# Performance work log

Measured on AMD Instinct MI355X. Metric: run time of the kernel, lower is better.

Reference implementation:

```python
import jax, jax.numpy as jnp
import numpy as np

N_BONDS = 16777216
N_ATOMS = 1048576
N_TYPES = 16


def setup_inputs() -> dict:
    key = jax.random.key(0)
    k1, k2, k3, k4, k5, k6 = jax.random.split(key, 6)
    # bond orders kept strictly positive so BO**p_be2 and its grad are finite
    bo_sigma = jax.random.uniform(k1, (N_BONDS,), jnp.float32, 0.05, 1.0)
    bo_pi = jax.random.uniform(k2, (N_BONDS,), jnp.float32, 0.05, 1.0)
    bo_pipi = jax.random.uniform(k3, (N_BONDS,), jnp.float32, 0.05, 1.0)
    bond_type = jax.random.randint(k4, (N_BONDS,), 0, N_TYPES, jnp.int32)
    atom_i = jax.random.randint(k5, (N_BONDS,), 0, N_ATOMS, jnp.int32)
    # columns: De_sigma, De_pi, De_pipi, p_be1, p_be2 (positive, O(1))
    bond_params = jax.random.uniform(k6, (N_TYPES, 5), jnp.float32, 0.1, 1.0)
    return {
        "bond_type": bond_type,
        "atom_i": atom_i,
        "bo_sigma": bo_sigma,
        "bo_pi": bo_pi,
        "bo_pipi": bo_pipi,
        "bond_params": bond_params,
        "n_atoms": N_ATOMS,
    }


def reference(bond_type, atom_i, bo_sigma, bo_pi, bo_pipi, bond_params, n_atoms):
    # Gather per-bond-type parameters: [E, 5]
    p = bond_params[bond_type]
    de_s, de_p, de_pp, p_be1, p_be2 = (p[:, 0], p[:, 1], p[:, 2], p[:, 3], p[:, 4])
    # ReaxFF bond energy per bond
    e_bond = (-de_s * bo_sigma * jnp.exp(p_be1 * (1.0 - bo_sigma ** p_be2))
              - de_p * bo_pi
              - de_pp * bo_pipi)
    # Scatter-reduce to per-atom energy
    e_atom = jax.ops.segment_sum(e_bond, atom_i, num_segments=n_atoms)
    return e_atom
```

## Files before the change

kernel.cpp:

```cpp
#include <hip/hip_runtime.h>


typedef float    f32x4 __attribute__((ext_vector_type(4)));
typedef int      i32x4 __attribute__((ext_vector_type(4)));
typedef unsigned u32x4 __attribute__((ext_vector_type(4)));
typedef unsigned u32;

#define NBUK   64
#define RANGEK 16384
#define SHIFTK 14
#define CB     8192
#define TB     256
#define PADQ   8u
#define SPLITS 4

__device__ __forceinline__ u32 f32_to_bf16_bits(float f) {
    u32 u = __float_as_uint(f);
    return ((u + 0x7FFFu + ((u >> 16) & 1u)) >> 16) & 0xFFFFu;
}

__global__ __launch_bounds__(TB, 4) void partition_kernel(
        const i32x4* __restrict__ bt, const i32x4* __restrict__ ai,
        const f32x4* __restrict__ bs_, const f32x4* __restrict__ bp_,
        const f32x4* __restrict__ bpp_, const float* __restrict__ bond_params,
        u32* __restrict__ gcur, u32* __restrict__ arena,
        float* __restrict__ out, u32 slab, int round_start) {
    __shared__ u32   sorted[CB];
    __shared__ u32   hist[4][NBUK];
    __shared__ u32   start_[NBUK], cur[NBUK], graw_[NBUK], ovf_[NBUK];
    __shared__ float4 sp_a[16];
    __shared__ float  sp_b[16];

    int tid = threadIdx.x, sb = blockIdx.x;
    ((u32*)hist)[tid] = 0u;
    if (tid < 16) {
        const float* p = bond_params + tid * 5;
        sp_a[tid] = make_float4(p[0], p[1], p[2], p[3]);
        sp_b[tid] = p[4];
    }
    __syncthreads();

    long base4 = ((long)round_start + (long)sb * CB) >> 2;
    int w = tid >> 6;
    i32x4 av[CB / (TB * 4)];
#pragma unroll
    for (int it = 0; it < CB / (TB * 4); ++it) {
        av[it] = ai[base4 + it * TB + tid];
        atomicAdd(&hist[w][(u32)av[it].x >> SHIFTK], 1u);
        atomicAdd(&hist[w][(u32)av[it].y >> SHIFTK], 1u);
        atomicAdd(&hist[w][(u32)av[it].z >> SHIFTK], 1u);
        atomicAdd(&hist[w][(u32)av[it].w >> SHIFTK], 1u);
    }
    __syncthreads();

    if (tid < 64) {
        u32 c = hist[0][tid] + hist[1][tid] + hist[2][tid] + hist[3][tid];
        u32 s = c;
#pragma unroll
        for (int off = 1; off < 64; off <<= 1) {
            u32 n = __shfl_up(s, off);
            if (tid >= off) s += n;
        }
        start_[tid] = s - c;
        cur[tid]    = s - c;
        u32 plen = (c + PADQ - 1u) & ~(PADQ - 1u);
        u32 g = atomicAdd(&gcur[tid], plen);
        graw_[tid] = g;
        ovf_[tid]  = (g + plen > slab) ? 1u : 0u;
    }
    __syncthreads();

#pragma unroll
    for (int it = 0; it < CB / (TB * 4); ++it) {
        long idx = base4 + it * TB + tid;
        i32x4 t  = bt[idx];
        f32x4 s  = bs_[idx];
        f32x4 p  = bp_[idx];
        f32x4 pp = bpp_[idx];
        i32x4 a  = av[it];
#pragma unroll
        for (int k = 0; k < 4; ++k) {
            u32 ak = (u32)a[k];
            float4 pa = sp_a[t[k]];
            float  pb = sp_b[t[k]];
            float pw = __powf(s[k], pb);
            float e  = -pa.x * s[k] * __expf(pa.w * (1.0f - pw))
                       - pa.y * p[k] - pa.z * pp[k];
            u32 b = ak >> SHIFTK;
            u32 pos = atomicAdd(&cur[b], 1u);
            sorted[pos] = ((ak & (RANGEK - 1u)) << 16) | f32_to_bf16_bits(e);
        }
    }
    __syncthreads();

    int lane = tid & 63;
    for (int b = w; b < NBUK; b += 4) {
        u32 ls = start_[b], len = cur[b] - ls;
        u32 plen = (len + PADQ - 1u) & ~(PADQ - 1u);
        u32 g = graw_[b];
        if (!ovf_[b]) {
            size_t base = (size_t)b * slab + g;
            for (u32 j = lane; j < plen; j += 64u)
                arena[base + j] = (j < len) ? sorted[ls + j] : 0u;
        } else {
            u32 z0 = g < slab ? g : slab;
            u32 z1 = (g + plen) < slab ? (g + plen) : slab;
            for (u32 j = z0 + lane; j < z1; j += 64u)
                arena[(size_t)b * slab + j] = 0u;
            for (u32 j = lane; j < len; j += 64u) {
                u32 e = sorted[ls + j];
                unsafeAtomicAdd(&out[((u32)b << SHIFTK) + (e >> 16)],
                                __uint_as_float((e & 0xFFFFu) << 16));
            }
        }
    }
}

__global__ __launch_bounds__(1024) void accum_kernel(
        const u32* __restrict__ arena, const u32* __restrict__ gcur,
        float* __restrict__ partials, u32 slab) {
    __shared__ float acc[RANGEK];
    int tid = threadIdx.x;
    int b = blockIdx.x >> 2, sp = blockIdx.x & 3;
    f32x4* a4 = (f32x4*)acc;
#pragma unroll
    for (int i = 0; i < RANGEK / 4 / 1024; ++i)
        a4[i * 1024 + tid] = (f32x4)(0.f);
    __syncthreads();
    u32 n = gcur[b];
    if (n > slab) n = slab;
    u32 nv = n >> 2;
    const u32x4* src = (const u32x4*)(arena + (size_t)b * slab);
    for (u32 j = (u32)sp * 1024u + tid; j < nv; j += 4096u) {
        u32x4 e = __builtin_nontemporal_load(&src[j]);
        atomicAdd(&acc[e.x >> 16], __uint_as_float((e.x & 0xFFFFu) << 16));
        atomicAdd(&acc[e.y >> 16], __uint_as_float((e.y & 0xFFFFu) << 16));
        atomicAdd(&acc[e.z >> 16], __uint_as_float((e.z & 0xFFFFu) << 16));
        atomicAdd(&acc[e.w >> 16], __uint_as_float((e.w & 0xFFFFu) << 16));
    }
    __syncthreads();
    f32x4* pr = (f32x4*)(partials + ((size_t)sp * NBUK + b) * RANGEK);
#pragma unroll
    for (int i = 0; i < RANGEK / 4 / 1024; ++i)
        pr[i * 1024 + tid] = a4[i * 1024 + tid];
}

__global__ __launch_bounds__(TB) void merge_kernel(
        const float* __restrict__ partials, float* __restrict__ out,
        int n_atoms) {
    int i = blockIdx.x * TB + threadIdx.x;
    const f32x4* p0 = (const f32x4*)partials;
    const f32x4* p1 = (const f32x4*)(partials + (size_t)n_atoms);
    const f32x4* p2 = (const f32x4*)(partials + 2 * (size_t)n_atoms);
    const f32x4* p3 = (const f32x4*)(partials + 3 * (size_t)n_atoms);
    f32x4* o4 = (f32x4*)out;
    o4[i] += p0[i] + p1[i] + p2[i] + p3[i];
}

__global__ __launch_bounds__(TB) void zero_kernel(f32x4* __restrict__ p, int n4) {
    int i = blockIdx.x * blockDim.x + threadIdx.x;
    if (i < n4) p[i] = (f32x4)(0.f);
}

__global__ __launch_bounds__(TB) void atomic_fallback_kernel(
        const i32x4* __restrict__ bt, const i32x4* __restrict__ ai,
        const f32x4* __restrict__ bs_, const f32x4* __restrict__ bp_,
        const f32x4* __restrict__ bpp_, const float* __restrict__ bond_params,
        float* __restrict__ out, int n4) {
    __shared__ float sp[80];
    if (threadIdx.x < 80) sp[threadIdx.x] = bond_params[threadIdx.x];
    __syncthreads();
    int i = blockIdx.x * blockDim.x + threadIdx.x;
    if (i >= n4) return;
    i32x4 t  = bt[i]; i32x4 a = ai[i];
    f32x4 s  = bs_[i]; f32x4 p = bp_[i]; f32x4 pp = bpp_[i];
#pragma unroll
    for (int k = 0; k < 4; ++k) {
        const float* pr = sp + t[k] * 5;
        float pw = __powf(s[k], pr[4]);
        float e  = -pr[0] * s[k] * __expf(pr[3] * (1.0f - pw))
                   - pr[1] * p[k] - pr[2] * pp[k];
        unsafeAtomicAdd(&out[a[k]], e);
    }
}

extern "C" void kernel_launch(void* const* d_in, const int* in_sizes, int n_in,
                              void* d_out, int out_size, void* d_ws, size_t ws_size,
                              hipStream_t stream) {
    const int*   bond_type   = (const int*)  d_in[0];
    const int*   atom_i      = (const int*)  d_in[1];
    const float* bo_sigma    = (const float*)d_in[2];
    const float* bo_pi       = (const float*)d_in[3];
    const float* bo_pipi     = (const float*)d_in[4];
    const float* bond_params = (const float*)d_in[5];
    float*       e_atom      = (float*)d_out;

    const int n_bonds = in_sizes[0];
    const int n_atoms = out_size;

    int cfg_nr = 0; u32 cfg_slab = 0;
    if (n_atoms == (NBUK << SHIFTK)) {
        const int cands[5] = {1, 2, 4, 8, 16};
        for (int ci = 0; ci < 5 && !cfg_nr; ++ci) {
            int r = cands[ci];
            if (n_bonds % (r * CB)) continue;
            long cpr = (long)n_bonds / r, nsb = cpr / CB;
            if (nsb < 256 || nsb > 8192) continue;
            u32 sl = (u32)((cpr / NBUK + nsb * 4 + 8192 + 7) & ~7L);
            size_t need = (size_t)NBUK * sl * 4
                        + 1024
                        + (size_t)SPLITS * n_atoms * 4;
            if (need <= ws_size) { cfg_nr = r; cfg_slab = sl; }
        }
    }

    if (cfg_nr) {
        const int NR = cfg_nr, cpr = n_bonds / NR, nsb = cpr / CB;
        u32*   arena    = (u32*)d_ws;
        u32*   gcur     = arena + (size_t)NBUK * cfg_slab;
        float* partials = (float*)(gcur + 256);
        int zn4 = n_atoms / 4;
        zero_kernel<<<(zn4 + TB - 1) / TB, TB, 0, stream>>>((f32x4*)e_atom, zn4);
        for (int r = 0; r < NR; ++r) {
            int rs = r * cpr;
            hipMemsetAsync(gcur, 0, NBUK * sizeof(u32), stream);
            partition_kernel<<<nsb, TB, 0, stream>>>(
                (const i32x4*)bond_type, (const i32x4*)atom_i,
                (const f32x4*)bo_sigma, (const f32x4*)bo_pi, (const f32x4*)bo_pipi,
                bond_params, gcur, arena, e_atom, cfg_slab, rs);
            accum_kernel<<<NBUK * SPLITS, 1024, 0, stream>>>(
                arena, gcur, partials, cfg_slab);
            merge_kernel<<<n_atoms / 4 / TB, TB, 0, stream>>>(
                partials, e_atom, n_atoms);
        }
    } else {
        int zn4 = n_atoms / 4;
        zero_kernel<<<(zn4 + TB - 1) / TB, TB, 0, stream>>>((f32x4*)e_atom, zn4);
        int n4 = n_bonds / 4;
        atomic_fallback_kernel<<<(n4 + TB - 1) / TB, TB, 0, stream>>>(
            (const i32x4*)bond_type, (const i32x4*)atom_i,
            (const f32x4*)bo_sigma, (const f32x4*)bo_pi, (const f32x4*)bo_pipi,
            bond_params, e_atom, n4);
    }
}
```

Measured before the change: 437.8 us.

## Split histogram into count kernel and replace partials merge with direct atomics

Moves the per-block bucket histogram into a separate count pass that stores u16 counts, so the partition kernel no longer keeps atom indices in registers across phases. Partition loads all inputs with nontemporal hints. The accumulate kernel atomically adds its shared-memory accumulator straight into the output, which removes the partials buffer and the merge kernel. The cost is reading atom_i twice and an extra launch; slab padding is also reduced.

```diff
diff --git a/kernel.cpp b/kernel.cpp
--- a/kernel.cpp
+++ b/kernel.cpp
@@ -5,6 +5,7 @@
 typedef int      i32x4 __attribute__((ext_vector_type(4)));
 typedef unsigned u32x4 __attribute__((ext_vector_type(4)));
 typedef unsigned u32;
+typedef unsigned short u16;
 
 #define NBUK   64
 #define RANGEK 16384
@@ -19,42 +20,48 @@
     return ((u + 0x7FFFu + ((u >> 16) & 1u)) >> 16) & 0xFFFFu;
 }
 
+__global__ __launch_bounds__(TB) void count_kernel(
+        const i32x4* __restrict__ atom_i, u16* __restrict__ counts,
+        int round_start) {
+    __shared__ u32 hist[4][NBUK];
+    int tid = threadIdx.x, w = tid >> 6;
+    ((u32*)hist)[tid] = 0u;
+    __syncthreads();
+    long base4 = ((long)round_start + (long)blockIdx.x * CB) >> 2;
+#pragma unroll
+    for (int it = 0; it < CB / (TB * 4); ++it) {
+        i32x4 a = __builtin_nontemporal_load(&atom_i[base4 + it * TB + tid]);
+        atomicAdd(&hist[w][(u32)a.x >> SHIFTK], 1u);
+        atomicAdd(&hist[w][(u32)a.y >> SHIFTK], 1u);
+        atomicAdd(&hist[w][(u32)a.z >> SHIFTK], 1u);
+        atomicAdd(&hist[w][(u32)a.w >> SHIFTK], 1u);
+    }
+    __syncthreads();
+    if (tid < NBUK)
+        counts[(size_t)blockIdx.x * NBUK + tid] =
+            (u16)(hist[0][tid] + hist[1][tid] + hist[2][tid] + hist[3][tid]);
+}
+
 __global__ __launch_bounds__(TB, 4) void partition_kernel(
         const i32x4* __restrict__ bt, const i32x4* __restrict__ ai,
         const f32x4* __restrict__ bs_, const f32x4* __restrict__ bp_,
         const f32x4* __restrict__ bpp_, const float* __restrict__ bond_params,
-        u32* __restrict__ gcur, u32* __restrict__ arena,
-        float* __restrict__ out, u32 slab, int round_start) {
+        const u16* __restrict__ counts, u32* __restrict__ gcur,
+        u32* __restrict__ arena, float* __restrict__ out,
+        u32 slab, int round_start) {
     __shared__ u32   sorted[CB];
-    __shared__ u32   hist[4][NBUK];
     __shared__ u32   start_[NBUK], cur[NBUK], graw_[NBUK], ovf_[NBUK];
     __shared__ float4 sp_a[16];
     __shared__ float  sp_b[16];
 
     int tid = threadIdx.x, sb = blockIdx.x;
-    ((u32*)hist)[tid] = 0u;
     if (tid < 16) {
         const float* p = bond_params + tid * 5;
         sp_a[tid] = make_float4(p[0], p[1], p[2], p[3]);
         sp_b[tid] = p[4];
     }
-    __syncthreads();
-
-    long base4 = ((long)round_start + (long)sb * CB) >> 2;
-    int w = tid >> 6;
-    i32x4 av[CB / (TB * 4)];
-#pragma unroll
-    for (int it = 0; it < CB / (TB * 4); ++it) {
-        av[it] = ai[base4 + it * TB + tid];
-        atomicAdd(&hist[w][(u32)av[it].x >> SHIFTK], 1u);
-        atomicAdd(&hist[w][(u32)av[it].y >> SHIFTK], 1u);
-        atomicAdd(&hist[w][(u32)av[it].z >> SHIFTK], 1u);
-        atomicAdd(&hist[w][(u32)av[it].w >> SHIFTK], 1u);
-    }
-    __syncthreads();
-
     if (tid < 64) {
-        u32 c = hist[0][tid] + hist[1][tid] + hist[2][tid] + hist[3][tid];
+        u32 c = counts[(size_t)sb * NBUK + tid];
         u32 s = c;
 #pragma unroll
         for (int off = 1; off < 64; off <<= 1) {
@@ -70,14 +77,15 @@
     }
     __syncthreads();
 
+    long base4 = ((long)round_start + (long)sb * CB) >> 2;
 #pragma unroll
     for (int it = 0; it < CB / (TB * 4); ++it) {
         long idx = base4 + it * TB + tid;
-        i32x4 t  = bt[idx];
-        f32x4 s  = bs_[idx];
-        f32x4 p  = bp_[idx];
-        f32x4 pp = bpp_[idx];
-        i32x4 a  = av[it];
+        i32x4 t  = __builtin_nontemporal_load(&bt[idx]);
+        i32x4 a  = __builtin_nontemporal_load(&ai[idx]);
+        f32x4 s  = __builtin_nontemporal_load(&bs_[idx]);
+        f32x4 p  = __builtin_nontemporal_load(&bp_[idx]);
+        f32x4 pp = __builtin_nontemporal_load(&bpp_[idx]);
 #pragma unroll
         for (int k = 0; k < 4; ++k) {
             u32 ak = (u32)a[k];
@@ -93,7 +101,7 @@
     }
     __syncthreads();
 
-    int lane = tid & 63;
+    int w = tid >> 6, lane = tid & 63;
     for (int b = w; b < NBUK; b += 4) {
         u32 ls = start_[b], len = cur[b] - ls;
         u32 plen = (len + PADQ - 1u) & ~(PADQ - 1u);
@@ -118,7 +126,7 @@
 
 __global__ __launch_bounds__(1024) void accum_kernel(
         const u32* __restrict__ arena, const u32* __restrict__ gcur,
-        float* __restrict__ partials, u32 slab) {
+        float* __restrict__ out, u32 slab) {
     __shared__ float acc[RANGEK];
     int tid = threadIdx.x;
     int b = blockIdx.x >> 2, sp = blockIdx.x & 3;
@@ -139,22 +147,10 @@
         atomicAdd(&acc[e.w >> 16], __uint_as_float((e.w & 0xFFFFu) << 16));
     }
     __syncthreads();
-    f32x4* pr = (f32x4*)(partials + ((size_t)sp * NBUK + b) * RANGEK);
-#pragma unroll
-    for (int i = 0; i < RANGEK / 4 / 1024; ++i)
-        pr[i * 1024 + tid] = a4[i * 1024 + tid];
-}
-
-__global__ __launch_bounds__(TB) void merge_kernel(
-        const float* __restrict__ partials, float* __restrict__ out,
-        int n_atoms) {
-    int i = blockIdx.x * TB + threadIdx.x;
-    const f32x4* p0 = (const f32x4*)partials;
-    const f32x4* p1 = (const f32x4*)(partials + (size_t)n_atoms);
-    const f32x4* p2 = (const f32x4*)(partials + 2 * (size_t)n_atoms);
-    const f32x4* p3 = (const f32x4*)(partials + 3 * (size_t)n_atoms);
-    f32x4* o4 = (f32x4*)out;
-    o4[i] += p0[i] + p1[i] + p2[i] + p3[i];
+    float* ob = out + ((size_t)b << SHIFTK);
+#pragma unroll
+    for (int i = 0; i < RANGEK / 1024; ++i)
+        unsafeAtomicAdd(&ob[i * 1024 + tid], acc[i * 1024 + tid]);
 }
 
 __global__ __launch_bounds__(TB) void zero_kernel(f32x4* __restrict__ p, int n4) {
@@ -206,32 +202,31 @@
             if (n_bonds % (r * CB)) continue;
             long cpr = (long)n_bonds / r, nsb = cpr / CB;
             if (nsb < 256 || nsb > 8192) continue;
-            u32 sl = (u32)((cpr / NBUK + nsb * 4 + 8192 + 7) & ~7L);
+            u32 sl = (u32)((cpr / NBUK + nsb * 4 + 4096 + 7) & ~7L);
             size_t need = (size_t)NBUK * sl * 4
                         + 1024
-                        + (size_t)SPLITS * n_atoms * 4;
+                        + (size_t)nsb * NBUK * 2;
             if (need <= ws_size) { cfg_nr = r; cfg_slab = sl; }
         }
     }
 
     if (cfg_nr) {
         const int NR = cfg_nr, cpr = n_bonds / NR, nsb = cpr / CB;
-        u32*   arena    = (u32*)d_ws;
-        u32*   gcur     = arena + (size_t)NBUK * cfg_slab;
-        float* partials = (float*)(gcur + 256);
+        u32* arena  = (u32*)d_ws;
+        u32* gcur   = arena + (size_t)NBUK * cfg_slab;
+        u16* counts = (u16*)(gcur + 256);
         int zn4 = n_atoms / 4;
         zero_kernel<<<(zn4 + TB - 1) / TB, TB, 0, stream>>>((f32x4*)e_atom, zn4);
         for (int r = 0; r < NR; ++r) {
             int rs = r * cpr;
             hipMemsetAsync(gcur, 0, NBUK * sizeof(u32), stream);
+            count_kernel<<<nsb, TB, 0, stream>>>((const i32x4*)atom_i, counts, rs);
             partition_kernel<<<nsb, TB, 0, stream>>>(
                 (const i32x4*)bond_type, (const i32x4*)atom_i,
                 (const f32x4*)bo_sigma, (const f32x4*)bo_pi, (const f32x4*)bo_pipi,
-                bond_params, gcur, arena, e_atom, cfg_slab, rs);
+                bond_params, counts, gcur, arena, e_atom, cfg_slab, rs);
             accum_kernel<<<NBUK * SPLITS, 1024, 0, stream>>>(
-                arena, gcur, partials, cfg_slab);
-            merge_kernel<<<n_atoms / 4 / TB, TB, 0, stream>>>(
-                partials, e_atom, n_atoms);
+                arena, gcur, e_atom, cfg_slab);
         }
     } else {
         int zn4 = n_atoms / 4;
```

New measurement: 436.2 us. No clear change (-0.4%).
